# Performance work log

Hardware: AMD Instinct MI355X
Metric: run time of the kernel (lower is better)

## Reference

```python
import jax, jax.numpy as jnp
import numpy as np

KS = 3      # kernel size
PAD = 1     # zero padding
STRIDE = 1
N = KS * KS # 9 sampling points per pixel


def _deform_conv(feature, offset, weight):
    """DeformConv2d: bilinear sample at learned offsets then 3x3 conv (no bias)."""
    b, c, h, w = feature.shape
    x = jnp.pad(feature, ((0, 0), (0, 0), (PAD, PAD), (PAD, PAD)))
    hp, wp = h + 2 * PAD, w + 2 * PAD
    dt = feature.dtype
    # p_n: kernel grid offsets, x(rows) first then y(cols) -> (2N,)
    rng = jnp.arange(-(KS - 1) // 2, (KS - 1) // 2 + 1, dtype=dt)
    pn_x, pn_y = jnp.meshgrid(rng, rng, indexing='ij')
    # p_0: base sampling grid starting at 1 (accounts for zero padding)
    p0_x, p0_y = jnp.meshgrid(jnp.arange(1, h + 1, dtype=dt),
                              jnp.arange(1, w + 1, dtype=dt), indexing='ij')
    # sampling locations p = p_0 + p_n + offset, split into x/y -> (b,h,w,N)
    off = jnp.transpose(offset, (0, 2, 3, 1))  # (b,h,w,2N)
    px = p0_x[None, :, :, None] + pn_x.reshape(-1)[None, None, None, :] + off[..., :N]
    py = p0_y[None, :, :, None] + pn_y.reshape(-1)[None, None, None, :] + off[..., N:]
    q_lt_x = jnp.clip(jnp.floor(px), 0, hp - 1)
    q_lt_y = jnp.clip(jnp.floor(py), 0, wp - 1)
    q_rb_x = jnp.clip(jnp.floor(px) + 1, 0, hp - 1)
    q_rb_y = jnp.clip(jnp.floor(py) + 1, 0, wp - 1)
    px = jnp.clip(px, 0, hp - 1)
    py = jnp.clip(py, 0, wp - 1)
    # bilinear weights for the 4 corners
    g_lt = (1 + (q_lt_x - px)) * (1 + (q_lt_y - py))
    g_rb = (1 - (q_rb_x - px)) * (1 - (q_rb_y - py))
    g_lb = (1 + (q_lt_x - px)) * (1 - (q_rb_y - py))
    g_rt = (1 - (q_rb_x - px)) * (1 + (q_lt_y - py))
    x_flat = x.reshape(b, c, hp * wp)

    def gather(qx, qy):
        idx = (qx * wp + qy).astype(jnp.int32).reshape(b, 1, -1)
        v = jnp.take_along_axis(x_flat, jnp.broadcast_to(idx, (b, c, h * w * N)), axis=2)
        return v.reshape(b, c, h, w, N)

    x_off = (g_lt[:, None] * gather(q_lt_x, q_lt_y)
             + g_rb[:, None] * gather(q_rb_x, q_rb_y)
             + g_lb[:, None] * gather(q_lt_x, q_rb_y)
             + g_rt[:, None] * gather(q_rb_x, q_lt_y))  # (b,c,h,w,N)
    # equivalent of _reshape_x_offset + conv(ks, stride=ks)
    x_off = x_off.reshape(b, c, h, w, KS, KS)
    return jnp.einsum('bchwij,ocij->bohw', x_off, weight)


def setup_inputs() -> dict:
    key = jax.random.key(0)
    k1, k2, k3 = jax.random.split(key, 3)
    B, C, H, W = 4, 256, 64, 64
    feature = jax.random.normal(k1, (B, C, H, W), dtype=jnp.float32)
    offset = jax.random.normal(k2, (B, 2 * N, H, W), dtype=jnp.float32)
    weight = jax.random.normal(k3, (C, C, KS, KS), dtype=jnp.float32) / np.sqrt(C * N)
    return {"feature": feature, "offset": offset, "weight": weight}


def reference(feature, offset, weight):
    f1 = jax.nn.relu(_deform_conv(feature, offset, weight))
    return jax.nn.relu(f1 + feature)
```

## Files before the change

kernel.cpp:

```cpp
#include <hip/hip_runtime.h>

#define HW    4096
#define J_TOT 16384
#define K_TOT 2304
#define C_CH  256

typedef unsigned short u16;
typedef unsigned int   u32;
typedef __attribute__((ext_vector_type(8))) short short8;
typedef __attribute__((ext_vector_type(4))) float f32x4;
typedef __attribute__((ext_vector_type(8))) unsigned short us8;

__device__ __forceinline__ float b2f(u16 u) { return __uint_as_float(((u32)u) << 16); }
__device__ __forceinline__ u16 f2b(float x) {
  u32 u = __float_as_uint(x);
  u += 0x7FFFu + ((u >> 16) & 1u);
  return (u16)(u >> 16);
}

__device__ __forceinline__ void gload_lds16(const u16* g, u16* l) {
  __builtin_amdgcn_global_load_lds(
      (__attribute__((address_space(1))) void*)(void*)g,
      (__attribute__((address_space(3))) void*)(void*)l, 16, 0, 0);
}

__global__ void k_detect(const u16* __restrict__ f, int* __restrict__ flag) {
  __shared__ int sh[256];
  int t = threadIdx.x;
  int hits = 0;
  for (int i = t; i < 2048; i += 256) {
    u16 u = f[2 * i];
    int e = (u >> 7) & 0xFF;
    hits += (e >= 100 && e <= 141) ? 1 : 0;
  }
  sh[t] = hits;
  __syncthreads();
  if (t == 0) {
    int s = 0;
    for (int i = 0; i < 256; i++) s += sh[i];
    flag[0] = (s > 1024) ? 1 : 0;
  }
}

__global__ void k_transpose(const void* __restrict__ featv, u16* __restrict__ ftr,
                            const int* __restrict__ flag) {
  __shared__ u16 tile[32][33];
  int isbf = *flag;
  int b = blockIdx.z;
  int hw0 = blockIdx.x << 5;
  int c0 = blockIdx.y << 5;
  int tx = threadIdx.x;
  int ty = threadIdx.y;
  if (isbf) {
    const u16* f = (const u16*)featv;
#pragma unroll
    for (int i = 0; i < 4; i++) {
      int c = c0 + ty + i * 8;
      tile[ty + i * 8][tx] = f[(((size_t)(b * C_CH + c)) << 12) + hw0 + tx];
    }
  } else {
    const float* f = (const float*)featv;
#pragma unroll
    for (int i = 0; i < 4; i++) {
      int c = c0 + ty + i * 8;
      tile[ty + i * 8][tx] = f2b(f[(((size_t)(b * C_CH + c)) << 12) + hw0 + tx]);
    }
  }
  __syncthreads();
#pragma unroll
  for (int i = 0; i < 4; i++) {
    int hw = hw0 + ty + i * 8;
    ftr[(((size_t)(b * HW + hw)) << 8) + c0 + tx] = tile[tx][ty + i * 8];
  }
}

__global__ void k_wconv(const void* __restrict__ wv, u16* __restrict__ Wr,
                        const int* __restrict__ flag) {
  int isbf = *flag;
  int idx = blockIdx.x * 256 + threadIdx.x;
  if (idx >= C_CH * K_TOT) return;
  int c = idx & 255;
  int n = (idx >> 8) % 9;
  int o = idx / K_TOT;
  int src = (o * 256 + c) * 9 + n;
  if (isbf) Wr[idx] = ((const u16*)wv)[src];
  else      Wr[idx] = f2b(((const float*)wv)[src]);
}

__global__ __launch_bounds__(256) void k_gather(const void* __restrict__ offv,
                                                const u16* __restrict__ ftr,
                                                u16* __restrict__ Xt,
                                                const int* __restrict__ flag) {
  __shared__ float gs[9][4][16];
  __shared__ int   isx[9][4][16];
  int isbf = *flag;
  int j0 = blockIdx.x << 4;
  int b = j0 >> 12;
  int hw0 = j0 & (HW - 1);
  int t = threadIdx.x;

  if (t < 144) {
    int p = t & 15, n = t >> 4;
    int hw = hw0 + p;
    int h = hw >> 6, w = hw & 63;
    size_t obi = (((size_t)(b * 18 + n)) << 12) + hw;
    float ox, oy;
    if (isbf) {
      const u16* po = (const u16*)offv;
      ox = b2f(po[obi]);
      oy = b2f(po[obi + (9u << 12)]);
    } else {
      const float* po = (const float*)offv;
      ox = po[obi];
      oy = po[obi + (9u << 12)];
    }
    int ki = n / 3, kj = n % 3;
    float px = (float)(h + ki) + ox;
    float py = (float)(w + kj) + oy;
    float fx = floorf(px), fy = floorf(py);
    float qltx = fminf(fmaxf(fx, 0.f), 65.f);
    float qlty = fminf(fmaxf(fy, 0.f), 65.f);
    float qrbx = fminf(fmaxf(fx + 1.f, 0.f), 65.f);
    float qrby = fminf(fmaxf(fy + 1.f, 0.f), 65.f);
    float pcx = fminf(fmaxf(px, 0.f), 65.f);
    float pcy = fminf(fmaxf(py, 0.f), 65.f);
    float dltx = 1.f + (qltx - pcx);
    float drbx = 1.f - (qrbx - pcx);
    float dlty = 1.f + (qlty - pcy);
    float drby = 1.f - (qrby - pcy);
    float g0 = dltx * dlty;
    float g1 = drbx * drby;
    float g2 = dltx * drby;
    float g3 = drbx * dlty;
    int x0 = (int)qltx, y0 = (int)qlty, x1 = (int)qrbx, y1 = (int)qrby;
    int v0 = (x0 >= 1 && x0 <= 64 && y0 >= 1 && y0 <= 64);
    int v1 = (x1 >= 1 && x1 <= 64 && y1 >= 1 && y1 <= 64);
    int v2 = (x0 >= 1 && x0 <= 64 && y1 >= 1 && y1 <= 64);
    int v3 = (x1 >= 1 && x1 <= 64 && y0 >= 1 && y0 <= 64);
    int base = b << 12;
    isx[n][0][p] = v0 ? ((base + ((x0 - 1) << 6) + (y0 - 1)) << 8) : 0;
    isx[n][1][p] = v1 ? ((base + ((x1 - 1) << 6) + (y1 - 1)) << 8) : 0;
    isx[n][2][p] = v2 ? ((base + ((x0 - 1) << 6) + (y1 - 1)) << 8) : 0;
    isx[n][3][p] = v3 ? ((base + ((x1 - 1) << 6) + (y0 - 1)) << 8) : 0;
    gs[n][0][p] = v0 ? g0 : 0.f;
    gs[n][1][p] = v1 ? g1 : 0.f;
    gs[n][2][p] = v2 ? g2 : 0.f;
    gs[n][3][p] = v3 ? g3 : 0.f;
  }
  __syncthreads();

  int p = t >> 4, cq = t & 15;
  size_t rowb = (size_t)(j0 + p) * K_TOT;
  int cA = cq * 8, cB = 128 + cq * 8;
  for (int n = 0; n < 9; n++) {
    float g0 = gs[n][0][p], g1 = gs[n][1][p], g2 = gs[n][2][p], g3 = gs[n][3][p];
    const u16* f0 = ftr + isx[n][0][p];
    const u16* f1 = ftr + isx[n][1][p];
    const u16* f2 = ftr + isx[n][2][p];
    const u16* f3 = ftr + isx[n][3][p];
    u16* dst = Xt + rowb + n * 256;
#pragma unroll
    for (int half = 0; half < 2; half++) {
      int c = half ? cB : cA;
      us8 r0 = *(const us8*)(f0 + c);
      us8 r1 = *(const us8*)(f1 + c);
      us8 r2 = *(const us8*)(f2 + c);
      us8 r3 = *(const us8*)(f3 + c);
      us8 ov;
#pragma unroll
      for (int i = 0; i < 8; i++) {
        float v = g0 * b2f(r0[i]) + g1 * b2f(r1[i]) + g2 * b2f(r2[i]) + g3 * b2f(r3[i]);
        ov[i] = f2b(v);
      }
      *(us8*)(dst + c) = ov;
    }
  }
}

#define NT 36

#define GEMM_STAGE(bufi)                                                     \
  do {                                                                       \
    gload_lds16(bsrc,  &Bs[bufi][wave * 512]);                               \
    gload_lds16(asrc0, &As[bufi][wave * 2048]);                              \
    gload_lds16(asrc1, &As[bufi][wave * 2048 + 512]);                        \
    gload_lds16(asrc2, &As[bufi][wave * 2048 + 1024]);                       \
    gload_lds16(asrc3, &As[bufi][wave * 2048 + 1536]);                       \
    bsrc += 64; asrc0 += 64; asrc1 += 64; asrc2 += 64; asrc3 += 64;          \
  } while (0)

#define GEMM_COMPUTE(bufi)                                                   \
  do {                                                                       \
    short8 af[2][2], bf[4][2];                                               \
    _Pragma("unroll")                                                        \
    for (int kk = 0; kk < 2; kk++) {                                         \
      int go = (((kk << 2) + lk) ^ swz) << 3;                                \
      _Pragma("unroll")                                                      \
      for (int oi = 0; oi < 2; oi++)                                         \
        af[oi][kk] = *(const short8*)(As[bufi] + (wave * 32 + oi * 16 + lr) * 64 + go); \
      _Pragma("unroll")                                                      \
      for (int ji = 0; ji < 4; ji++)                                         \
        bf[ji][kk] = *(const short8*)(Bs[bufi] + (ji * 16 + lr) * 64 + go);  \
    }                                                                        \
    __builtin_amdgcn_s_setprio(1);                                           \
    _Pragma("unroll")                                                        \
    for (int kk = 0; kk < 2; kk++)                                           \
      _Pragma("unroll")                                                      \
      for (int oi = 0; oi < 2; oi++)                                         \
        _Pragma("unroll")                                                    \
        for (int ji = 0; ji < 4; ji++)                                       \
          acc[oi][ji] = __builtin_amdgcn_mfma_f32_16x16x32_bf16(             \
              af[oi][kk], bf[ji][kk], acc[oi][ji], 0, 0, 0);                 \
    __builtin_amdgcn_s_setprio(0);                                           \
  } while (0)

__global__ __launch_bounds__(512) void k_gemm(const u16* __restrict__ Wr,
                                              const u16* __restrict__ Xt,
                                              const void* __restrict__ featv,
                                              void* __restrict__ outv,
                                              const int* __restrict__ flag) {
  __shared__ u16 Bs[3][64 * 64];
  __shared__ u16 As[3][256 * 64];
  int isbf = *flag;
  asm volatile("" :: "s"(isbf));
  int jb = blockIdx.x << 6;
  int t = threadIdx.x;
  int wave = t >> 6, lane = t & 63;
  int lr = lane & 15, lk = lane >> 4;
  int swz = lr & 7;

  f32x4 acc[2][4];
  f32x4 zero = {0.f, 0.f, 0.f, 0.f};
#pragma unroll
  for (int i = 0; i < 2; i++)
#pragma unroll
    for (int j = 0; j < 4; j++) acc[i][j] = zero;

  int rb = lane >> 3;
  int cs = ((lane & 7) ^ rb) << 3;
  const u16* bsrc  = Xt + (size_t)(jb + wave * 8 + rb) * K_TOT + cs;
  const u16* asrc0 = Wr + (size_t)(wave * 32 +  0 + rb) * K_TOT + cs;
  const u16* asrc1 = Wr + (size_t)(wave * 32 +  8 + rb) * K_TOT + cs;
  const u16* asrc2 = Wr + (size_t)(wave * 32 + 16 + rb) * K_TOT + cs;
  const u16* asrc3 = Wr + (size_t)(wave * 32 + 24 + rb) * K_TOT + cs;

  GEMM_STAGE(0);
  GEMM_STAGE(1);
  asm volatile("s_waitcnt vmcnt(5)" ::: "memory");
  __builtin_amdgcn_s_barrier();

  int cb = 0, sb = 2;
  for (int tt = 0; tt < NT - 2; ++tt) {
    GEMM_STAGE(sb);
    GEMM_COMPUTE(cb);
    asm volatile("s_waitcnt vmcnt(5)" ::: "memory");
    __builtin_amdgcn_s_barrier();
    cb = (cb + 1 == 3) ? 0 : cb + 1;
    sb = (sb + 1 == 3) ? 0 : sb + 1;
  }
  GEMM_COMPUTE(cb);
  asm volatile("s_waitcnt vmcnt(0)" ::: "memory");
  __builtin_amdgcn_s_barrier();
  cb = (cb + 1 == 3) ? 0 : cb + 1;
  GEMM_COMPUTE(cb);

  int lq = lane >> 4;
#pragma unroll
  for (int oi = 0; oi < 2; oi++) {
#pragma unroll
    for (int ji = 0; ji < 4; ji++) {
      int j = jb + ji * 16 + lr;
      int bb_ = j >> 12, hw = j & (HW - 1);
      int o0 = wave * 32 + oi * 16 + lq * 4;
#pragma unroll
      for (int r = 0; r < 4; r++) {
        size_t oidx = (((size_t)(bb_ * C_CH + o0 + r)) << 12) + hw;
        float v = acc[oi][ji][r];
        v = fmaxf(v, 0.f);
        float ft = isbf ? b2f(((const u16*)featv)[oidx]) : ((const float*)featv)[oidx];
        v = fmaxf(v + ft, 0.f);
        if (isbf) ((u16*)outv)[oidx] = f2b(v);
        else      ((float*)outv)[oidx] = v;
      }
    }
  }
}

extern "C" void kernel_launch(void* const* d_in, const int* in_sizes, int n_in,
                              void* d_out, int out_size, void* d_ws, size_t ws_size,
                              hipStream_t stream) {
  const void* feat = d_in[0];
  const void* offs = d_in[1];
  const void* wght = d_in[2];

  const size_t off_flag = 0;
  const size_t off_wr   = 256;
  const size_t off_ftr  = off_wr + (size_t)1179648;
  const size_t off_xt   = off_ftr + (size_t)8388608;
  const size_t need     = off_xt + (size_t)75497472;
  if (ws_size < need) return;

  char* ws = (char*)d_ws;
  int* flag = (int*)(ws + off_flag);
  u16* Wr   = (u16*)(ws + off_wr);
  u16* ftr  = (u16*)(ws + off_ftr);
  u16* Xt   = (u16*)(ws + off_xt);

  k_detect<<<1, 256, 0, stream>>>((const u16*)feat, flag);
  k_transpose<<<dim3(128, 8, 4), dim3(32, 8), 0, stream>>>(feat, ftr, flag);
  k_wconv<<<K_TOT, 256, 0, stream>>>(wght, Wr, flag);
  k_gather<<<J_TOT / 16, 256, 0, stream>>>(offs, ftr, Xt, flag);
  k_gemm<<<J_TOT / 64, 512, 0, stream>>>(Wr, Xt, feat, d_out, flag);
}
```

Before: 145.0 us.

## Fuse bilinear gather into GEMM producer, eliminating im2col buffer

Folds the deformable bilinear sampling into the GEMM kernel. Each block computes the sampling indices and weights for its 64 pixels into LDS, then builds each K-tile of the B operand directly in LDS from the transposed features while the weight tile streams in by DMA. This removes the 75 MB Xt intermediate, with its global write and re-read, and one kernel launch. In exchange the GEMM drops from a triple-buffered to a double-buffered pipeline, and the gather loads sit on the critical path of every K step, which may expose latency.

```diff
diff --git a/kernel.cpp b/kernel.cpp
--- a/kernel.cpp
+++ b/kernel.cpp
@@ -87,20 +87,86 @@
   else      Wr[idx] = f2b(((const float*)wv)[src]);
 }
 
-__global__ __launch_bounds__(256) void k_gather(const void* __restrict__ offv,
-                                                const u16* __restrict__ ftr,
-                                                u16* __restrict__ Xt,
-                                                const int* __restrict__ flag) {
-  __shared__ float gs[9][4][16];
-  __shared__ int   isx[9][4][16];
+#define NT 36
+
+#define A_DMA(bufi)                                                          \
+  do {                                                                       \
+    gload_lds16(asrc0, &As[bufi][wave * 2048]);                              \
+    gload_lds16(asrc1, &As[bufi][wave * 2048 + 512]);                        \
+    gload_lds16(asrc2, &As[bufi][wave * 2048 + 1024]);                       \
+    gload_lds16(asrc3, &As[bufi][wave * 2048 + 1536]);                       \
+    asrc0 += 64; asrc1 += 64; asrc2 += 64; asrc3 += 64;                      \
+  } while (0)
+
+#define PLOAD(tile)                                                          \
+  do {                                                                       \
+    int np = (tile) >> 2, c0 = ((tile) & 3) << 6;                            \
+    w0 = gs[np][0][pp]; w1 = gs[np][1][pp];                                  \
+    w2 = gs[np][2][pp]; w3 = gs[np][3][pp];                                  \
+    q0 = *(const us8*)(ftr + isx[np][0][pp] + c0 + cb8);                     \
+    q1 = *(const us8*)(ftr + isx[np][1][pp] + c0 + cb8);                     \
+    q2 = *(const us8*)(ftr + isx[np][2][pp] + c0 + cb8);                     \
+    q3 = *(const us8*)(ftr + isx[np][3][pp] + c0 + cb8);                     \
+  } while (0)
+
+#define PFIN(bufi)                                                           \
+  do {                                                                       \
+    us8 ov;                                                                  \
+    _Pragma("unroll")                                                        \
+    for (int i = 0; i < 8; i++) {                                            \
+      float v = w0 * b2f(q0[i]) + w1 * b2f(q1[i]) +                          \
+                w2 * b2f(q2[i]) + w3 * b2f(q3[i]);                           \
+      ov[i] = f2b(v);                                                        \
+    }                                                                        \
+    *(us8*)(&Bs[bufi][bofs]) = ov;                                           \
+  } while (0)
+
+#define GEMM_COMPUTE(bufi)                                                   \
+  do {                                                                       \
+    short8 af[2][2], bf[4][2];                                               \
+    _Pragma("unroll")                                                        \
+    for (int kk = 0; kk < 2; kk++) {                                         \
+      int go = (((kk << 2) + lk) ^ swz) << 3;                                \
+      _Pragma("unroll")                                                      \
+      for (int oi = 0; oi < 2; oi++)                                         \
+        af[oi][kk] = *(const short8*)(As[bufi] + (wave * 32 + oi * 16 + lr) * 64 + go); \
+      _Pragma("unroll")                                                      \
+      for (int ji = 0; ji < 4; ji++)                                         \
+        bf[ji][kk] = *(const short8*)(Bs[bufi] + (ji * 16 + lr) * 64 + go);  \
+    }                                                                        \
+    __builtin_amdgcn_s_setprio(1);                                           \
+    _Pragma("unroll")                                                        \
+    for (int kk = 0; kk < 2; kk++)                                           \
+      _Pragma("unroll")                                                      \
+      for (int oi = 0; oi < 2; oi++)                                         \
+        _Pragma("unroll")                                                    \
+        for (int ji = 0; ji < 4; ji++)                                       \
+          acc[oi][ji] = __builtin_amdgcn_mfma_f32_16x16x32_bf16(             \
+              af[oi][kk], bf[ji][kk], acc[oi][ji], 0, 0, 0);                 \
+    __builtin_amdgcn_s_setprio(0);                                           \
+  } while (0)
+
+__global__ __launch_bounds__(512) void k_gemm(const u16* __restrict__ Wr,
+                                              const u16* __restrict__ ftr,
+                                              const void* __restrict__ offv,
+                                              const void* __restrict__ featv,
+                                              void* __restrict__ outv,
+                                              const int* __restrict__ flag) {
+  __shared__ u16 As[2][256 * 64];
+  __shared__ u16 Bs[2][64 * 64];
+  __shared__ float gs[9][4][64];
+  __shared__ int   isx[9][4][64];
   int isbf = *flag;
-  int j0 = blockIdx.x << 4;
+  int j0 = blockIdx.x << 6;
   int b = j0 >> 12;
   int hw0 = j0 & (HW - 1);
   int t = threadIdx.x;
-
-  if (t < 144) {
-    int p = t & 15, n = t >> 4;
+  int wave = t >> 6, lane = t & 63;
+  int lr = lane & 15, lk = lane >> 4;
+  int swz = lr & 7;
+
+  for (int e = t; e < 576; e += 512) {
+    int n = e >> 6, p = e & 63;
     int hw = hw0 + p;
     int h = hw >> 6, w = hw & 63;
     size_t obi = (((size_t)(b * 18 + n)) << 12) + hw;
@@ -147,87 +213,6 @@
     gs[n][2][p] = v2 ? g2 : 0.f;
     gs[n][3][p] = v3 ? g3 : 0.f;
   }
-  __syncthreads();
-
-  int p = t >> 4, cq = t & 15;
-  size_t rowb = (size_t)(j0 + p) * K_TOT;
-  int cA = cq * 8, cB = 128 + cq * 8;
-  for (int n = 0; n < 9; n++) {
-    float g0 = gs[n][0][p], g1 = gs[n][1][p], g2 = gs[n][2][p], g3 = gs[n][3][p];
-    const u16* f0 = ftr + isx[n][0][p];
-    const u16* f1 = ftr + isx[n][1][p];
-    const u16* f2 = ftr + isx[n][2][p];
-    const u16* f3 = ftr + isx[n][3][p];
-    u16* dst = Xt + rowb + n * 256;
-#pragma unroll
-    for (int half = 0; half < 2; half++) {
-      int c = half ? cB : cA;
-      us8 r0 = *(const us8*)(f0 + c);
-      us8 r1 = *(const us8*)(f1 + c);
-      us8 r2 = *(const us8*)(f2 + c);
-      us8 r3 = *(const us8*)(f3 + c);
-      us8 ov;
-#pragma unroll
-      for (int i = 0; i < 8; i++) {
-        float v = g0 * b2f(r0[i]) + g1 * b2f(r1[i]) + g2 * b2f(r2[i]) + g3 * b2f(r3[i]);
-        ov[i] = f2b(v);
-      }
-      *(us8*)(dst + c) = ov;
-    }
-  }
-}
-
-#define NT 36
-
-#define GEMM_STAGE(bufi)                                                     \
-  do {                                                                       \
-    gload_lds16(bsrc,  &Bs[bufi][wave * 512]);                               \
-    gload_lds16(asrc0, &As[bufi][wave * 2048]);                              \
-    gload_lds16(asrc1, &As[bufi][wave * 2048 + 512]);                        \
-    gload_lds16(asrc2, &As[bufi][wave * 2048 + 1024]);                       \
-    gload_lds16(asrc3, &As[bufi][wave * 2048 + 1536]);                       \
-    bsrc += 64; asrc0 += 64; asrc1 += 64; asrc2 += 64; asrc3 += 64;          \
-  } while (0)
-
-#define GEMM_COMPUTE(bufi)                                                   \
-  do {                                                                       \
-    short8 af[2][2], bf[4][2];                                               \
-    _Pragma("unroll")                                                        \
-    for (int kk = 0; kk < 2; kk++) {                                         \
-      int go = (((kk << 2) + lk) ^ swz) << 3;                                \
-      _Pragma("unroll")                                                      \
-      for (int oi = 0; oi < 2; oi++)                                         \
-        af[oi][kk] = *(const short8*)(As[bufi] + (wave * 32 + oi * 16 + lr) * 64 + go); \
-      _Pragma("unroll")                                                      \
-      for (int ji = 0; ji < 4; ji++)                                         \
-        bf[ji][kk] = *(const short8*)(Bs[bufi] + (ji * 16 + lr) * 64 + go);  \
-    }                                                                        \
-    __builtin_amdgcn_s_setprio(1);                                           \
-    _Pragma("unroll")                                                        \
-    for (int kk = 0; kk < 2; kk++)                                           \
-      _Pragma("unroll")                                                      \
-      for (int oi = 0; oi < 2; oi++)                                         \
-        _Pragma("unroll")                                                    \
-        for (int ji = 0; ji < 4; ji++)                                       \
-          acc[oi][ji] = __builtin_amdgcn_mfma_f32_16x16x32_bf16(             \
-              af[oi][kk], bf[ji][kk], acc[oi][ji], 0, 0, 0);                 \
-    __builtin_amdgcn_s_setprio(0);                                           \
-  } while (0)
-
-__global__ __launch_bounds__(512) void k_gemm(const u16* __restrict__ Wr,
-                                              const u16* __restrict__ Xt,
-                                              const void* __restrict__ featv,
-                                              void* __restrict__ outv,
-                                              const int* __restrict__ flag) {
-  __shared__ u16 Bs[3][64 * 64];
-  __shared__ u16 As[3][256 * 64];
-  int isbf = *flag;
-  asm volatile("" :: "s"(isbf));
-  int jb = blockIdx.x << 6;
-  int t = threadIdx.x;
-  int wave = t >> 6, lane = t & 63;
-  int lr = lane & 15, lk = lane >> 4;
-  int swz = lr & 7;
 
   f32x4 acc[2][4];
   f32x4 zero = {0.f, 0.f, 0.f, 0.f};
@@ -238,38 +223,41 @@
 
   int rb = lane >> 3;
   int cs = ((lane & 7) ^ rb) << 3;
-  const u16* bsrc  = Xt + (size_t)(jb + wave * 8 + rb) * K_TOT + cs;
   const u16* asrc0 = Wr + (size_t)(wave * 32 +  0 + rb) * K_TOT + cs;
   const u16* asrc1 = Wr + (size_t)(wave * 32 +  8 + rb) * K_TOT + cs;
   const u16* asrc2 = Wr + (size_t)(wave * 32 + 16 + rb) * K_TOT + cs;
   const u16* asrc3 = Wr + (size_t)(wave * 32 + 24 + rb) * K_TOT + cs;
 
-  GEMM_STAGE(0);
-  GEMM_STAGE(1);
-  asm volatile("s_waitcnt vmcnt(5)" ::: "memory");
-  __builtin_amdgcn_s_barrier();
-
-  int cb = 0, sb = 2;
-  for (int tt = 0; tt < NT - 2; ++tt) {
-    GEMM_STAGE(sb);
-    GEMM_COMPUTE(cb);
-    asm volatile("s_waitcnt vmcnt(5)" ::: "memory");
-    __builtin_amdgcn_s_barrier();
-    cb = (cb + 1 == 3) ? 0 : cb + 1;
-    sb = (sb + 1 == 3) ? 0 : sb + 1;
-  }
-  GEMM_COMPUTE(cb);
-  asm volatile("s_waitcnt vmcnt(0)" ::: "memory");
-  __builtin_amdgcn_s_barrier();
-  cb = (cb + 1 == 3) ? 0 : cb + 1;
-  GEMM_COMPUTE(cb);
+  int pp = t >> 3, cg = t & 7;
+  int bofs = pp * 64 + ((cg ^ (pp & 7)) << 3);
+  int cb8 = cg << 3;
+
+  __syncthreads();
+
+  us8 q0, q1, q2, q3;
+  float w0, w1, w2, w3;
+
+  PLOAD(0);
+  A_DMA(0);
+  PFIN(0);
+  __syncthreads();
+
+  for (int tt = 0; tt < NT - 1; ++tt) {
+    int cbuf = tt & 1, nbuf = cbuf ^ 1;
+    PLOAD(tt + 1);
+    A_DMA(nbuf);
+    GEMM_COMPUTE(cbuf);
+    PFIN(nbuf);
+    __syncthreads();
+  }
+  GEMM_COMPUTE((NT - 1) & 1);
 
   int lq = lane >> 4;
 #pragma unroll
   for (int oi = 0; oi < 2; oi++) {
 #pragma unroll
     for (int ji = 0; ji < 4; ji++) {
-      int j = jb + ji * 16 + lr;
+      int j = j0 + ji * 16 + lr;
       int bb_ = j >> 12, hw = j & (HW - 1);
       int o0 = wave * 32 + oi * 16 + lq * 4;
 #pragma unroll
@@ -296,19 +284,16 @@
   const size_t off_flag = 0;
   const size_t off_wr   = 256;
   const size_t off_ftr  = off_wr + (size_t)1179648;
-  const size_t off_xt   = off_ftr + (size_t)8388608;
-  const size_t need     = off_xt + (size_t)75497472;
+  const size_t need     = off_ftr + (size_t)8388608;
   if (ws_size < need) return;
 
   char* ws = (char*)d_ws;
   int* flag = (int*)(ws + off_flag);
   u16* Wr   = (u16*)(ws + off_wr);
   u16* ftr  = (u16*)(ws + off_ftr);
-  u16* Xt   = (u16*)(ws + off_xt);
 
   k_detect<<<1, 256, 0, stream>>>((const u16*)feat, flag);
   k_transpose<<<dim3(128, 8, 4), dim3(32, 8), 0, stream>>>(feat, ftr, flag);
   k_wconv<<<K_TOT, 256, 0, stream>>>(wght, Wr, flag);
-  k_gather<<<J_TOT / 16, 256, 0, stream>>>(offs, ftr, Xt, flag);
-  k_gemm<<<J_TOT / 64, 512, 0, stream>>>(Wr, Xt, feat, d_out, flag);
-}
+  k_gemm<<<J_TOT / 64, 512, 0, stream>>>(Wr, ftr, offs, feat, d_out, flag);
+}
```

After: 140.8 us. 1.03x faster.
